# Kernel tuning notes

Measured on AMD Instinct MI355X. Metric: run time of the kernel, lower is better.

The kernel has to match this reference:

```python
import jax, jax.numpy as jnp
import numpy as np

C = 5.0          # tanh clamp constant (args.c, non-trainable)
B, N, R, D = 4, 16, 64, 256  # batch, block_num, block_len, word_dim
NEG = -1e9


def setup_inputs() -> dict:
    key = jax.random.key(0)
    ks = iter(jax.random.split(key, 80))

    def W(i, o):
        # xavier-like init (torch stores (out,in); we store (in,out) and use x @ W)
        return jax.random.normal(next(ks), (i, o), jnp.float32) * np.float32(np.sqrt(2.0 / (i + o)))

    def bvec(d):
        return jax.random.normal(next(ks), (d,), jnp.float32) * 0.01

    inp = {"x": jax.random.normal(next(ks), (B, N, R, D), jnp.float32)}
    for p in ("fw", "bw"):
        inp[f"fcW_{p}"] = W(D, D);  inp[f"fcb_{p}"] = bvec(D)
        inp[f"mW1_{p}"] = W(D, D);  inp[f"mW2_{p}"] = W(D, D);  inp[f"mb_{p}"] = bvec(D)
        inp[f"s2tW1_{p}"] = W(D, D); inp[f"s2tb1_{p}"] = bvec(D)
        inp[f"s2tW_{p}"] = W(D, D);  inp[f"s2tb_{p}"] = bvec(D)
        inp[f"gW1_{p}"] = W(D, D);  inp[f"gW2_{p}"] = W(D, D);  inp[f"gb_{p}"] = bvec(D)
        inp[f"fW1_{p}"] = W(3 * D, D); inp[f"fb1_{p}"] = bvec(D)
        inp[f"fW2_{p}"] = W(3 * D, D); inp[f"fb2_{p}"] = bvec(D)
    return inp


def _mSA(x, W1, W2, b, fw):
    # x: (..., L, d) -> (..., L, d). Additive per-feature attention with strict
    # triangular mask. fw: token i attends to j > i (last row zeroed);
    # bw: token i attends to j < i (first row zeroed). Matches the torch
    # -inf mask + narrow + zero-pad construction exactly.
    L = x.shape[-2]
    xi = (x @ W1)[..., :, None, :]                 # (..., L, 1, d)
    xj = (x @ W2)[..., None, :, :]                 # (..., 1, L, d)
    f = C * jnp.tanh((xi + xj + b) / C)            # (..., i, j, d)
    i = jnp.arange(L)[:, None]
    j = jnp.arange(L)[None, :]
    allowed = (j > i) if fw else (j < i)           # (L, L)
    scores = jnp.where(allowed[..., None], f, NEG)
    att = jax.nn.softmax(scores, axis=-2)          # softmax over j
    rowvalid = (jnp.arange(L) < L - 1) if fw else (jnp.arange(L) > 0)
    att = att * rowvalid[:, None, None].astype(x.dtype)
    return jnp.einsum('...ijd,...jd->...id', att, x)


def _s2t(x, W1, b1, Wo, bo):
    # source2token self-attention: (..., L, d) -> (..., d)
    f = jax.nn.relu(x @ W1 + b1)
    a = jax.nn.softmax(f @ Wo + bo, axis=-2)
    return jnp.sum(a * x, axis=-2)


def _mblosa(x, mW1, mW2, mb, s2tW1, s2tb1, s2tW, s2tb,
            gW1, gW2, gb, fW1, fb1, fW2, fb2, fw):
    Bb, n, r, d = x.shape
    h = _mSA(x, mW1, mW2, mb, fw)                  # (B, n, r, d) intra-block
    v = _s2t(h, s2tW1, s2tb1, s2tW, s2tb)          # (B, n, d)    block summary
    o = _mSA(v, mW1, mW2, mb, fw)                  # (B, n, d)    inter-block
    G = jax.nn.sigmoid(o @ gW1 + v @ gW2 + gb)
    e = G * o + (1.0 - G) * v                      # (B, n, d)
    # torch: cat of e[i] repeated r times, then narrow(1, 0, n)
    idx = jnp.arange(n) // r
    E = e[:, idx]                                  # (B, n, d)
    # torch: flatten blocks then narrow(1, 0, n) (faithful to source)
    xf = x.reshape(Bb, n * r, d)[:, :n]
    hf = h.reshape(Bb, n * r, d)[:, :n]
    cat = jnp.concatenate([xf, hf, E], axis=-1)    # (B, n, 3d)
    fusion = jax.nn.relu(cat @ fW1 + fb1)
    Gf = jax.nn.sigmoid(cat @ fW2 + fb2)
    return Gf * fusion + (1.0 - Gf) * xf           # (B, n, d)


def reference(x,
              fcW_fw, fcb_fw, mW1_fw, mW2_fw, mb_fw, s2tW1_fw, s2tb1_fw,
              s2tW_fw, s2tb_fw, gW1_fw, gW2_fw, gb_fw, fW1_fw, fb1_fw,
              fW2_fw, fb2_fw,
              fcW_bw, fcb_bw, mW1_bw, mW2_bw, mb_bw, s2tW1_bw, s2tb1_bw,
              s2tW_bw, s2tb_bw, gW1_bw, gW2_bw, gb_bw, fW1_bw, fb1_bw,
              fW2_bw, fb2_bw):
    in_fw = jax.nn.relu(x @ fcW_fw + fcb_fw)
    in_bw = jax.nn.relu(x @ fcW_bw + fcb_bw)
    u_fw = _mblosa(in_fw, mW1_fw, mW2_fw, mb_fw, s2tW1_fw, s2tb1_fw,
                   s2tW_fw, s2tb_fw, gW1_fw, gW2_fw, gb_fw,
                   fW1_fw, fb1_fw, fW2_fw, fb2_fw, True)
    u_bw = _mblosa(in_bw, mW1_bw, mW2_bw, mb_bw, s2tW1_bw, s2tb1_bw,
                   s2tW_bw, s2tb_bw, gW1_bw, gW2_bw, gb_bw,
                   fW1_bw, fb1_bw, fW2_bw, fb2_bw, False)
    return jnp.concatenate([u_fw, u_bw], axis=-1)  # (B, n, 2d)
```

## Files before the change

### kernel.cpp

```cpp
#include <hip/hip_runtime.h>
#include <hip/hip_bf16.h>

typedef __hip_bfloat16 BF16;
typedef __attribute__((ext_vector_type(8))) short short8;
typedef __attribute__((ext_vector_type(4))) float f32x4;

#define MFMA_B16(a,b,c) __builtin_amdgcn_mfma_f32_16x16x32_bf16((a),(b),(c),0,0,0)

#if __has_builtin(__builtin_amdgcn_exp2f)
#define EXP2F(x) __builtin_amdgcn_exp2f(x)
#else
#define EXP2F(x) __expf(0.6931471805599453f * (x))
#endif

__device__ __forceinline__ short f2bs(float f){ BF16 h = __float2bfloat16(f); return *(short*)&h; }
__device__ __forceinline__ float bs2f(short s){ BF16 h = *(BF16*)&s; return __bfloat162float(h); }

struct SrcPack { const float* s[10]; };

__global__ __launch_bounds__(256) void prep_k(SrcPack p, short* __restrict__ Oh,
                                              short* __restrict__ Ol)
{
    __shared__ float s[64][65];
    const float* W = p.s[blockIdx.y];
    short* oh = Oh + (size_t)blockIdx.y * 65536;
    short* ol = Ol + (size_t)blockIdx.y * 65536;
    int tr = (blockIdx.x >> 2) * 64, tc = (blockIdx.x & 3) * 64;
    #pragma unroll
    for (int i = 0; i < 16; i++) {
        int e = threadIdx.x + i * 256;
        int r = e >> 6, c = e & 63;
        s[c][r] = W[(size_t)(tr + r) * 256 + tc + c];
    }
    __syncthreads();
    #pragma unroll
    for (int i = 0; i < 16; i++) {
        int e = threadIdx.x + i * 256;
        int c2 = e >> 6, r2 = e & 63;
        float v = s[c2][r2];
        short hi = f2bs(v);
        short lo = f2bs(v - bs2f(hi));
        size_t oi = (size_t)(tc + c2) * 256 + tr + r2;
        oh[oi] = hi;
        ol[oi] = lo;
    }
}

template<int AM, int OM, int RELU, int BS>
__device__ __forceinline__ void gemm_body(const void* __restrict__ A0,
    const void* __restrict__ Alo,
    const short* __restrict__ Wh, const short* __restrict__ Wl,
    const float* __restrict__ bias, void* __restrict__ O0, void* __restrict__ O1,
    int row0, int col0)
{
    constexpr int LDK = 72;
    __shared__ short sAh[64 * LDK];
    __shared__ short sAl[(AM == 0) ? 8 : 64 * LDK];
    __shared__ short sBh[64 * LDK];
    __shared__ short sBl[BS ? 8 : 64 * LDK];
    int tid = threadIdx.x;
    int w = tid >> 6, l = tid & 63;
    int m = l & 15, q = l >> 4;
    int sr = w * 16 + m;

    f32x4 acc[4];
    #pragma unroll
    for (int cf = 0; cf < 4; cf++) acc[cf] = (f32x4)(0.f);

    for (int kh = 0; kh < 4; kh++) {
        int kbase = kh * 64;
        #pragma unroll
        for (int i = 0; i < 2; i++) {
            int kl = q * 8 + 32 * i;
            size_t gofs = (size_t)(row0 + sr) * 256 + kbase + kl;
            if (AM == 1) {
                const float* src = (const float*)A0 + gofs;
                float4 f0 = *(const float4*)src;
                float4 f1 = *(const float4*)(src + 4);
                short8 vh, vl;
                float tmp[8] = {f0.x, f0.y, f0.z, f0.w, f1.x, f1.y, f1.z, f1.w};
                #pragma unroll
                for (int j = 0; j < 8; j++) {
                    vh[j] = f2bs(tmp[j]);
                    vl[j] = f2bs(tmp[j] - bs2f(vh[j]));
                }
                *(short8*)&sAh[sr * LDK + kl] = vh;
                *(short8*)&sAl[sr * LDK + kl] = vl;
            } else if (AM == 2) {
                *(short8*)&sAh[sr * LDK + kl] = *(const short8*)((const short*)A0 + gofs);
                *(short8*)&sAl[sr * LDK + kl] = *(const short8*)((const short*)Alo + gofs);
            } else {
                *(short8*)&sAh[sr * LDK + kl] = *(const short8*)((const short*)A0 + gofs);
            }
            size_t gofsB = (size_t)(col0 + sr) * 256 + kbase + kl;
            *(short8*)&sBh[sr * LDK + kl] = *(const short8*)(Wh + gofsB);
            if (!BS)
                *(short8*)&sBl[sr * LDK + kl] = *(const short8*)(Wl + gofsB);
        }
        __syncthreads();
        #pragma unroll
        for (int ch = 0; ch < 2; ch++) {
            int k = ch * 32 + q * 8;
            short8 ah = *(const short8*)&sAh[(w * 16 + m) * LDK + k];
            short8 al = (AM != 0) ? *(const short8*)&sAl[(w * 16 + m) * LDK + k] : ah;
            #pragma unroll
            for (int cf = 0; cf < 4; cf++) {
                short8 bh = *(const short8*)&sBh[(cf * 16 + m) * LDK + k];
                acc[cf] = MFMA_B16(ah, bh, acc[cf]);
                if (!BS) {
                    short8 bl = *(const short8*)&sBl[(cf * 16 + m) * LDK + k];
                    acc[cf] = MFMA_B16(ah, bl, acc[cf]);
                }
                if (AM != 0)
                    acc[cf] = MFMA_B16(al, bh, acc[cf]);
            }
        }
        __syncthreads();
    }
    #pragma unroll
    for (int cf = 0; cf < 4; cf++) {
        int col = col0 + cf * 16 + m;
        float bv = bias ? bias[col] : 0.f;
        #pragma unroll
        for (int r = 0; r < 4; r++) {
            int row = row0 + w * 16 + q * 4 + r;
            float v = acc[cf][r] + bv;
            if (RELU) v = fmaxf(v, 0.f);
            size_t oi = (size_t)row * 256 + col;
            if (OM == 0) {
                ((float*)O0)[oi] = v;
            } else if (OM == 1) {
                ((short*)O0)[oi] = f2bs(v);
            } else {
                short hi = f2bs(v);
                ((short*)O0)[oi] = hi;
                ((short*)O1)[oi] = f2bs(v - bs2f(hi));
            }
        }
    }
}

struct GDir { const void* A0; const void* Al; const short* Wh; const short* Wl;
              const float* bias; void* O0; void* O1; };

template<int AM, int OM, int RELU, int BS>
__global__ __launch_bounds__(256) void gemm_k(GDir p0, GDir p1)
{
    GDir p = blockIdx.z ? p1 : p0;
    gemm_body<AM, OM, RELU, BS>(p.A0, p.Al, p.Wh, p.Wl, p.bias, p.O0, p.O1,
                                blockIdx.x * 64, blockIdx.y * 64);
}

struct G2Dir { const float* A; const short* W1h; const short* W1l;
               const short* W2h; const short* W2l; const float* b2;
               float* C1; float* C2; };

__global__ __launch_bounds__(256) void gemm2s_k(G2Dir p0)
{
    G2Dir p = p0;
    int y = blockIdx.y;
    const short* Wh = (y < 4) ? p.W1h : p.W2h;
    const short* Wl = (y < 4) ? p.W1l : p.W2l;
    void* C = (y < 4) ? (void*)p.C1 : (void*)p.C2;
    const float* bias = (y < 4) ? nullptr : p.b2;
    gemm_body<1, 0, 0, 0>(p.A, nullptr, Wh, Wl, bias, C, nullptr, 0, (y & 3) * 64);
}

struct MbloDir { const short* Ah;
                 const short* W1h; const short* W2h;
                 const float* mb; short* Hh; int fw; };

__global__ __launch_bounds__(512) void mblo_k(MbloDir p0, MbloDir p1)
{
    __shared__ char smraw[33536] __attribute__((aligned(16)));
    short* gAh  = (short*)smraw;
    short* gB1h = gAh + 4608;
    short* gB2h = gAh + 9216;
    float* aP   = (float*)smraw;
    unsigned int* aQX = (unsigned int*)(smraw + 16896);

    const float KLN = -0.06931471805599453f;

    MbloDir p = blockIdx.z ? p1 : p0;
    int tid = threadIdx.x;
    int w = tid >> 6, l = tid & 63;
    int m = l & 15, q = l >> 4;
    int rh = w >> 1;
    int cb = (w & 1) * 2;
    int bn = blockIdx.x >> 1, ipar = blockIdx.x & 1;
    int row0 = bn * 64, d0 = blockIdx.y * 64;
    int srow = tid >> 3;
    int skl  = (tid & 7) * 8;

    f32x4 acc1[2], acc2[2];
    #pragma unroll
    for (int cf = 0; cf < 2; cf++) { acc1[cf] = (f32x4)(0.f); acc2[cf] = (f32x4)(0.f); }

    for (int kh = 0; kh < 4; kh++) {
        int kbase = kh * 64;
        size_t ga = (size_t)(row0 + srow) * 256 + kbase + skl;
        *(short8*)&gAh[srow * 72 + skl] = *(const short8*)(p.Ah + ga);
        size_t gb = (size_t)(d0 + srow) * 256 + kbase + skl;
        *(short8*)&gB1h[srow * 72 + skl] = *(const short8*)(p.W1h + gb);
        *(short8*)&gB2h[srow * 72 + skl] = *(const short8*)(p.W2h + gb);
        __syncthreads();
        #pragma unroll
        for (int ch = 0; ch < 2; ch++) {
            int k = ch * 32 + q * 8;
            short8 ah = *(const short8*)&gAh[(rh * 16 + m) * 72 + k];
            #pragma unroll
            for (int cf = 0; cf < 2; cf++) {
                int bofs = ((cb + cf) * 16 + m) * 72 + k;
                short8 b1 = *(const short8*)&gB1h[bofs];
                acc1[cf] = MFMA_B16(ah, b1, acc1[cf]);
                short8 b2 = *(const short8*)&gB2h[bofs];
                acc2[cf] = MFMA_B16(ah, b2, acc2[cf]);
            }
        }
        __syncthreads();
    }
    short* sQX = (short*)aQX;
    #pragma unroll
    for (int cf = 0; cf < 2; cf++) {
        int col = (cb + cf) * 16 + m;
        float mbv = p.mb[d0 + col];
        #pragma unroll
        for (int r = 0; r < 4; r++) {
            int row = rh * 16 + q * 4 + r;
            aP[row * 66 + col] = __expf(0.4f * acc1[cf][r]) * KLN;
            sQX[col * 130 + 2 * row] = f2bs(__expf(0.4f * (acc2[cf][r] + mbv)));
        }
    }
    {
        size_t gx = (size_t)(row0 + srow) * 256 + d0 + skl;
        short8 xh = *(const short8*)(p.Ah + gx);
        #pragma unroll
        for (int t = 0; t < 8; t++)
            sQX[(skl + t) * 130 + 2 * srow + 1] = xh[t];
    }
    __syncthreads();
    const unsigned int* lane_qx = &aQX[l * 65];
    #pragma unroll
    for (int t8 = 0; t8 < 4; t8++) {
        int i = ipar + 2 * (w + 8 * t8);
        float Pp = aP[i * 66 + l];
        int js = p.fw ? (i + 1) : 0;
        int je = p.fw ? 64 : i;
        float den0 = 0.f, den1 = 0.f, num0 = 0.f, num1 = 0.f;
        int j = js;
        for (; j + 4 <= je; j += 4) {
            unsigned int u0 = lane_qx[j];
            unsigned int u1 = lane_qx[j + 1];
            unsigned int u2 = lane_qx[j + 2];
            unsigned int u3 = lane_qx[j + 3];
            float q0 = bs2f((short)(u0 & 0xffff)), x0 = bs2f((short)(u0 >> 16));
            float q1 = bs2f((short)(u1 & 0xffff)), x1 = bs2f((short)(u1 >> 16));
            float q2 = bs2f((short)(u2 & 0xffff)), x2 = bs2f((short)(u2 >> 16));
            float q3 = bs2f((short)(u3 & 0xffff)), x3 = bs2f((short)(u3 >> 16));
            float w0 = EXP2F(__builtin_amdgcn_rcpf(fmaf(Pp, q0, KLN)));
            float w1 = EXP2F(__builtin_amdgcn_rcpf(fmaf(Pp, q1, KLN)));
            float w2 = EXP2F(__builtin_amdgcn_rcpf(fmaf(Pp, q2, KLN)));
            float w3 = EXP2F(__builtin_amdgcn_rcpf(fmaf(Pp, q3, KLN)));
            den0 += w0; num0 = fmaf(w0, x0, num0);
            den1 += w1; num1 = fmaf(w1, x1, num1);
            den0 += w2; num0 = fmaf(w2, x2, num0);
            den1 += w3; num1 = fmaf(w3, x3, num1);
        }
        for (; j < je; j++) {
            unsigned int u0 = lane_qx[j];
            float q0 = bs2f((short)(u0 & 0xffff)), x0 = bs2f((short)(u0 >> 16));
            float wgt = EXP2F(__builtin_amdgcn_rcpf(fmaf(Pp, q0, KLN)));
            den0 += wgt; num0 = fmaf(wgt, x0, num0);
        }
        float den = den0 + den1, num = num0 + num1;
        bool valid = p.fw ? (i < 63) : (i > 0);
        float out = valid ? (num * __builtin_amdgcn_rcpf(den)) : 0.f;
        p.Hh[(size_t)(row0 + i) * 256 + d0 + l] = f2bs(out);
    }
}

struct PoolDir { const short* T1; const short* Wh; const float* bias;
                 const short* Hh; float* V; };

__global__ __launch_bounds__(256) void s2t_pool_k(PoolDir p0, PoolDir p1)
{
    __shared__ char smraw[37888] __attribute__((aligned(16)));
    short* gAh = (short*)smraw;
    short* gBh = gAh + 4608;
    float* aL = (float*)smraw;
    float* aH = aL + 4352;
    float* rm = aL + 8704;
    float* rd = aL + 8960;
    float* rn = aL + 9216;

    PoolDir p = blockIdx.z ? p1 : p0;
    int tid = threadIdx.x;
    int w = tid >> 6, l = tid & 63;
    int m = l & 15, q = l >> 4;
    int sr = w * 16 + m;
    int row0 = blockIdx.x * 64, d0 = blockIdx.y * 64;

    f32x4 acc[4];
    #pragma unroll
    for (int cf = 0; cf < 4; cf++) acc[cf] = (f32x4)(0.f);

    for (int kh = 0; kh < 4; kh++) {
        int kbase = kh * 64;
        #pragma unroll
        for (int i = 0; i < 2; i++) {
            int kl = q * 8 + 32 * i;
            *(short8*)&gAh[sr * 72 + kl] =
                *(const short8*)(p.T1 + (size_t)(row0 + sr) * 256 + kbase + kl);
            *(short8*)&gBh[sr * 72 + kl] =
                *(const short8*)(p.Wh + (size_t)(d0 + sr) * 256 + kbase + kl);
        }
        __syncthreads();
        #pragma unroll
        for (int ch = 0; ch < 2; ch++) {
            int k = ch * 32 + q * 8;
            short8 ah = *(const short8*)&gAh[(w * 16 + m) * 72 + k];
            #pragma unroll
            for (int cf = 0; cf < 4; cf++) {
                short8 bh = *(const short8*)&gBh[(cf * 16 + m) * 72 + k];
                acc[cf] = MFMA_B16(ah, bh, acc[cf]);
            }
        }
        __syncthreads();
    }
    #pragma unroll
    for (int cf = 0; cf < 4; cf++) {
        int col = cf * 16 + m;
        float bv = p.bias[d0 + col];
        #pragma unroll
        for (int r = 0; r < 4; r++) {
            int row = w * 16 + q * 4 + r;
            aL[row * 68 + col] = acc[cf][r] + bv;
        }
    }
    #pragma unroll
    for (int it = 0; it < 2; it++) {
        int e = tid + it * 256;
        int j = e >> 3, d8 = (e & 7) * 8;
        short8 xh = *(const short8*)(p.Hh + (size_t)(row0 + j) * 256 + d0 + d8);
        #pragma unroll
        for (int t = 0; t < 8; t++)
            aH[j * 68 + d8 + t] = bs2f(xh[t]);
    }
    __syncthreads();
    int dl = tid & 63, rq = tid >> 6;
    float mx = -1e30f, den = 0.f, num = 0.f;
    #pragma unroll
    for (int rr = 0; rr < 16; rr++) {
        int r = rq * 16 + rr;
        float lv = aL[r * 68 + dl];
        float hv = aH[r * 68 + dl];
        if (lv > mx) {
            float sc = __expf(mx - lv);
            den *= sc; num *= sc; mx = lv;
        }
        float wgt = __expf(lv - mx);
        den += wgt; num += wgt * hv;
    }
    rm[rq * 64 + dl] = mx; rd[rq * 64 + dl] = den; rn[rq * 64 + dl] = num;
    __syncthreads();
    if (rq == 0) {
        float M = fmaxf(fmaxf(rm[dl], rm[64 + dl]), fmaxf(rm[128 + dl], rm[192 + dl]));
        float D = 0.f, Nn = 0.f;
        #pragma unroll
        for (int k = 0; k < 4; k++) {
            float sc = __expf(rm[k * 64 + dl] - M);
            D += rd[k * 64 + dl] * sc;
            Nn += rn[k * 64 + dl] * sc;
        }
        p.V[(size_t)blockIdx.x * 256 + d0 + dl] = Nn / D;
    }
}

struct GateDir { const float* vW1; const float* vW2; const float* V;
                 const float* gW1; const float* gW2; const float* gb;
                 float* E0; int fw; };

__global__ __launch_bounds__(256) void attn2gate_k(GateDir p0, GateDir p1)
{
    GateDir p = blockIdx.z ? p1 : p0;
    __shared__ float so[256], sv[256], red[4][64];
    int b = blockIdx.x, k = threadIdx.x;
    float o = 0.f;
    if (p.fw) {
        float qv = p.vW1[(size_t)(b * 16) * 256 + k];
        float den = 0.f, num = 0.f;
        for (int j = 1; j < 16; j++) {
            float z = (qv + p.vW2[(size_t)(b * 16 + j) * 256 + k]) * 0.2f;
            float e2 = __expf(2.f * z);
            float t = 1.f - 2.f / (e2 + 1.f);
            float wgt = __expf(5.f * t);
            den += wgt; num += wgt * p.V[(size_t)(b * 16 + j) * 256 + k];
        }
        o = num / den;
    }
    so[k] = o;
    sv[k] = p.V[(size_t)(b * 16) * 256 + k];
    __syncthreads();
    int c = k & 63, ks = k >> 6;
    int gc = blockIdx.y * 64 + c;
    float acc = 0.f;
    int k0 = ks * 64;
    #pragma unroll 8
    for (int kk = 0; kk < 64; kk++) {
        int kx = k0 + kk;
        acc += so[kx] * p.gW1[(size_t)kx * 256 + gc] + sv[kx] * p.gW2[(size_t)kx * 256 + gc];
    }
    red[ks][c] = acc;
    __syncthreads();
    if (ks == 0) {
        float a = red[0][c] + red[1][c] + red[2][c] + red[3][c] + p.gb[gc];
        float G = 1.f / (1.f + __expf(-a));
        p.E0[b * 256 + gc] = G * so[gc] + (1.f - G) * sv[gc];
    }
}

struct FuseDir { const short* INh; const short* Hh;
                 const float* E0; const float* fW1; const float* fb1;
                 const float* fW2; const float* fb2; };

__global__ __launch_bounds__(256) void fusion_k(FuseDir p0, FuseDir p1, float* __restrict__ out)
{
    FuseDir p = blockIdx.z ? p1 : p0;
    __shared__ float cat[768];
    __shared__ float red1[4][64], red2[4][64];
    int bt = blockIdx.x, b = bt >> 4, t = bt & 15;
    int c = threadIdx.x & 63, ks = threadIdx.x >> 6;
    int gc = blockIdx.y * 64 + c;
    size_t xrow = ((size_t)b * 1024 + t) * 256;
    cat[threadIdx.x]       = bs2f(p.INh[xrow + threadIdx.x]);
    cat[256 + threadIdx.x] = bs2f(p.Hh[xrow + threadIdx.x]);
    cat[512 + threadIdx.x] = p.E0[b * 256 + threadIdx.x];
    __syncthreads();
    float a1 = 0.f, a2 = 0.f;
    int k0 = ks * 192;
    #pragma unroll 8
    for (int kk = 0; kk < 192; kk++) {
        int k = k0 + kk;
        float cv = cat[k];
        a1 += cv * p.fW1[(size_t)k * 256 + gc];
        a2 += cv * p.fW2[(size_t)k * 256 + gc];
    }
    red1[ks][c] = a1; red2[ks][c] = a2;
    __syncthreads();
    if (ks == 0) {
        float s1 = red1[0][c] + red1[1][c] + red1[2][c] + red1[3][c] + p.fb1[gc];
        float s2 = red2[0][c] + red2[1][c] + red2[2][c] + red2[3][c] + p.fb2[gc];
        float fus = fmaxf(s1, 0.f);
        float Gf = 1.f / (1.f + __expf(-s2));
        float u = Gf * fus + (1.f - Gf) * cat[gc];
        out[((size_t)(b * 16 + t)) * 512 + (size_t)blockIdx.z * 256 + gc] = u;
    }
}

extern "C" void kernel_launch(void* const* d_in, const int* in_sizes, int n_in,
                              void* d_out, int out_size, void* d_ws, size_t ws_size,
                              hipStream_t stream)
{
    const float* x = (const float*)d_in[0];
    char* base = (char*)d_ws;
    auto alloc = [&](size_t bytes){ void* r = base; base += (bytes + 255) & ~255ULL; return r; };
    short* inH = (short*)alloc(2 * 1048576 * 2);
    short* hH  = (short*)alloc(2 * 1048576 * 2);
    short* t1  = (short*)alloc(2 * 1048576 * 2);
    short* wtH = (short*)alloc(10 * 65536 * 2);
    short* wtL = (short*)alloc(10 * 65536 * 2);
    float* v   = (float*)alloc(2 * 16384 * 4);
    float* vW1 = (float*)alloc(16384 * 4);
    float* vW2 = (float*)alloc(16384 * 4);
    float* E0  = (float*)alloc(2 * 1024 * 4);

    SrcPack sp;
    const int src_idx[5] = {0, 2, 3, 5, 7};
    for (int p = 0; p < 2; p++)
        for (int i = 0; i < 5; i++)
            sp.s[p * 5 + i] = (const float*)d_in[1 + p * 16 + src_idx[i]];
    prep_k<<<dim3(16, 10), 256, 0, stream>>>(sp, wtH, wtL);

    GDir fc[2], s2t1[2];
    MbloDir mbd[2];
    PoolDir pld[2];
    G2Dir g2d;
    GateDir gtd[2];
    FuseDir fsd[2];
    for (int p = 0; p < 2; p++) {
        int bi = 1 + p * 16;
        const float* fcb   = (const float*)d_in[bi + 1];
        const float* mb    = (const float*)d_in[bi + 4];
        const float* s2tb1 = (const float*)d_in[bi + 6];
        const float* s2tb  = (const float*)d_in[bi + 8];
        size_t po = (size_t)p * 1048576;
        const short* W0h = wtH + (size_t)(p * 5 + 0) * 65536, *W0l = wtL + (size_t)(p * 5 + 0) * 65536;
        const short* W1h = wtH + (size_t)(p * 5 + 1) * 65536, *W1l = wtL + (size_t)(p * 5 + 1) * 65536;
        const short* W2h = wtH + (size_t)(p * 5 + 2) * 65536, *W2l = wtL + (size_t)(p * 5 + 2) * 65536;
        const short* W3h = wtH + (size_t)(p * 5 + 3) * 65536;
        const short* W4h = wtH + (size_t)(p * 5 + 4) * 65536;

        fc[p]   = { x, nullptr, W0h, W0l, fcb, inH + po, nullptr };
        mbd[p]  = { inH + po, W1h, W2h, mb, hH + po, (p == 0) };
        s2t1[p] = { hH + po, nullptr, W3h, nullptr, s2tb1, t1 + po, nullptr };
        pld[p]  = { t1 + po, W4h, s2tb, hH + po, v + p * 16384 };
        if (p == 0) g2d = { v, W1h, W1l, W2h, W2l, mb, vW1, vW2 };
        gtd[p]  = { vW1, vW2, v + p * 16384,
                    (const float*)d_in[bi + 9], (const float*)d_in[bi + 10],
                    (const float*)d_in[bi + 11], E0 + p * 1024, (p == 0) };
        fsd[p]  = { inH + po, hH + po, E0 + p * 1024,
                    (const float*)d_in[bi + 12], (const float*)d_in[bi + 13],
                    (const float*)d_in[bi + 14], (const float*)d_in[bi + 15] };
    }

    gemm_k<1, 1, 1, 0><<<dim3(64, 4, 2), 256, 0, stream>>>(fc[0], fc[1]);
    mblo_k<<<dim3(128, 4, 2), 512, 0, stream>>>(mbd[0], mbd[1]);
    gemm_k<0, 1, 1, 1><<<dim3(64, 4, 2), 256, 0, stream>>>(s2t1[0], s2t1[1]);
    s2t_pool_k<<<dim3(64, 4, 2), 256, 0, stream>>>(pld[0], pld[1]);
    gemm2s_k<<<dim3(1, 8, 1), 256, 0, stream>>>(g2d);
    attn2gate_k<<<dim3(4, 4, 2), 256, 0, stream>>>(gtd[0], gtd[1]);
    fusion_k<<<dim3(64, 4, 2), 256, 0, stream>>>(fsd[0], fsd[1], (float*)d_out);
}
```

Baseline: 200.8 us.

## Fuse s2t GEMM into pooling kernel and fold inter-block projections into gate kernel

The s2t first GEMM (ReLU) is now computed per 64-row block inside the pooling kernel, with T1 kept in shared memory, so the t1 global buffer and one launch go away. Each block recomputes T1 for its two output column chunks, so that GEMM runs twice across blockIdx.y. The separate gemm2s kernel that projected V through W1/W2 is removed. Those projections are now computed in fp32 directly inside attn2gate using the original weights, which cuts two launches in total and adds redundant per-block scalar FMA work.

```diff
diff --git a/kernel.cpp b/kernel.cpp
--- a/kernel.cpp
+++ b/kernel.cpp
@@ -149,21 +149,6 @@
     GDir p = blockIdx.z ? p1 : p0;
     gemm_body<AM, OM, RELU, BS>(p.A0, p.Al, p.Wh, p.Wl, p.bias, p.O0, p.O1,
                                 blockIdx.x * 64, blockIdx.y * 64);
-}
-
-struct G2Dir { const float* A; const short* W1h; const short* W1l;
-               const short* W2h; const short* W2l; const float* b2;
-               float* C1; float* C2; };
-
-__global__ __launch_bounds__(256) void gemm2s_k(G2Dir p0)
-{
-    G2Dir p = p0;
-    int y = blockIdx.y;
-    const short* Wh = (y < 4) ? p.W1h : p.W2h;
-    const short* Wl = (y < 4) ? p.W1l : p.W2l;
-    void* C = (y < 4) ? (void*)p.C1 : (void*)p.C2;
-    const float* bias = (y < 4) ? nullptr : p.b2;
-    gemm_body<1, 0, 0, 0>(p.A, nullptr, Wh, Wl, bias, C, nullptr, 0, (y & 3) * 64);
 }
 
 struct MbloDir { const short* Ah;
@@ -279,141 +264,222 @@
     }
 }
 
-struct PoolDir { const short* T1; const short* Wh; const float* bias;
-                 const short* Hh; float* V; };
-
-__global__ __launch_bounds__(256) void s2t_pool_k(PoolDir p0, PoolDir p1)
-{
-    __shared__ char smraw[37888] __attribute__((aligned(16)));
-    short* gAh = (short*)smraw;
-    short* gBh = gAh + 4608;
-    float* aL = (float*)smraw;
-    float* aH = aL + 4352;
-    float* rm = aL + 8704;
-    float* rd = aL + 8960;
-    float* rn = aL + 9216;
-
-    PoolDir p = blockIdx.z ? p1 : p0;
+struct S2TDir { const short* Hh; const short* W3h; const float* b1;
+                const short* W4h; const float* b2; float* V; };
+
+__global__ __launch_bounds__(512) void s2t_fused_k(S2TDir p0, S2TDir p1)
+{
+    __shared__ char smraw[79872] __attribute__((aligned(16)));
+    short* sT1 = (short*)smraw;
+    short* gA  = (short*)(smraw + 33792);
+    short* gB  = (short*)(smraw + 43008);
+    short* gB2 = (short*)(smraw + 33792);
+    float* aL  = (float*)(smraw + 43008);
+    float* rm  = (float*)(smraw + 60416);
+    float* rd  = rm + 512;
+    float* rn  = rm + 1024;
+
+    S2TDir p = blockIdx.z ? p1 : p0;
     int tid = threadIdx.x;
     int w = tid >> 6, l = tid & 63;
     int m = l & 15, q = l >> 4;
-    int sr = w * 16 + m;
-    int row0 = blockIdx.x * 64, d0 = blockIdx.y * 64;
-
-    f32x4 acc[4];
-    #pragma unroll
-    for (int cf = 0; cf < 4; cf++) acc[cf] = (f32x4)(0.f);
-
+    int row0 = blockIdx.x * 64;
+    int strip = w >> 1, chalf = w & 1;
+    int srow = tid >> 3, skl = (tid & 7) * 8;
+
+    f32x4 acc1[8];
+    #pragma unroll
+    for (int cf = 0; cf < 8; cf++) acc1[cf] = (f32x4)(0.f);
     for (int kh = 0; kh < 4; kh++) {
         int kbase = kh * 64;
-        #pragma unroll
-        for (int i = 0; i < 2; i++) {
-            int kl = q * 8 + 32 * i;
-            *(short8*)&gAh[sr * 72 + kl] =
-                *(const short8*)(p.T1 + (size_t)(row0 + sr) * 256 + kbase + kl);
-            *(short8*)&gBh[sr * 72 + kl] =
-                *(const short8*)(p.Wh + (size_t)(d0 + sr) * 256 + kbase + kl);
+        *(short8*)&gA[srow * 72 + skl] =
+            *(const short8*)(p.Hh + (size_t)(row0 + srow) * 256 + kbase + skl);
+        int bn = tid >> 1;
+        #pragma unroll
+        for (int i = 0; i < 4; i++) {
+            int kseg = (tid & 1) * 32 + i * 8;
+            *(short8*)&gB[bn * 72 + kseg] =
+                *(const short8*)(p.W3h + (size_t)bn * 256 + kbase + kseg);
         }
         __syncthreads();
         #pragma unroll
         for (int ch = 0; ch < 2; ch++) {
             int k = ch * 32 + q * 8;
-            short8 ah = *(const short8*)&gAh[(w * 16 + m) * 72 + k];
-            #pragma unroll
-            for (int cf = 0; cf < 4; cf++) {
-                short8 bh = *(const short8*)&gBh[(cf * 16 + m) * 72 + k];
-                acc[cf] = MFMA_B16(ah, bh, acc[cf]);
-            }
-        }
-        __syncthreads();
-    }
-    #pragma unroll
-    for (int cf = 0; cf < 4; cf++) {
-        int col = cf * 16 + m;
-        float bv = p.bias[d0 + col];
+            short8 ah = *(const short8*)&gA[(strip * 16 + m) * 72 + k];
+            #pragma unroll
+            for (int cf = 0; cf < 8; cf++) {
+                short8 bh = *(const short8*)&gB[(chalf * 128 + cf * 16 + m) * 72 + k];
+                acc1[cf] = MFMA_B16(ah, bh, acc1[cf]);
+            }
+        }
+        __syncthreads();
+    }
+    #pragma unroll
+    for (int cf = 0; cf < 8; cf++) {
+        int col = chalf * 128 + cf * 16 + m;
+        float bv = p.b1[col];
         #pragma unroll
         for (int r = 0; r < 4; r++) {
-            int row = w * 16 + q * 4 + r;
-            aL[row * 68 + col] = acc[cf][r] + bv;
-        }
-    }
-    #pragma unroll
-    for (int it = 0; it < 2; it++) {
-        int e = tid + it * 256;
-        int j = e >> 3, d8 = (e & 7) * 8;
-        short8 xh = *(const short8*)(p.Hh + (size_t)(row0 + j) * 256 + d0 + d8);
-        #pragma unroll
-        for (int t = 0; t < 8; t++)
-            aH[j * 68 + d8 + t] = bs2f(xh[t]);
-    }
-    __syncthreads();
-    int dl = tid & 63, rq = tid >> 6;
-    float mx = -1e30f, den = 0.f, num = 0.f;
-    #pragma unroll
-    for (int rr = 0; rr < 16; rr++) {
-        int r = rq * 16 + rr;
-        float lv = aL[r * 68 + dl];
-        float hv = aH[r * 68 + dl];
-        if (lv > mx) {
-            float sc = __expf(mx - lv);
-            den *= sc; num *= sc; mx = lv;
-        }
-        float wgt = __expf(lv - mx);
-        den += wgt; num += wgt * hv;
-    }
-    rm[rq * 64 + dl] = mx; rd[rq * 64 + dl] = den; rn[rq * 64 + dl] = num;
-    __syncthreads();
-    if (rq == 0) {
-        float M = fmaxf(fmaxf(rm[dl], rm[64 + dl]), fmaxf(rm[128 + dl], rm[192 + dl]));
-        float D = 0.f, Nn = 0.f;
-        #pragma unroll
-        for (int k = 0; k < 4; k++) {
-            float sc = __expf(rm[k * 64 + dl] - M);
-            D += rd[k * 64 + dl] * sc;
-            Nn += rn[k * 64 + dl] * sc;
-        }
-        p.V[(size_t)blockIdx.x * 256 + d0 + dl] = Nn / D;
-    }
-}
-
-struct GateDir { const float* vW1; const float* vW2; const float* V;
-                 const float* gW1; const float* gW2; const float* gb;
-                 float* E0; int fw; };
-
-__global__ __launch_bounds__(256) void attn2gate_k(GateDir p0, GateDir p1)
-{
-    GateDir p = blockIdx.z ? p1 : p0;
-    __shared__ float so[256], sv[256], red[4][64];
-    int b = blockIdx.x, k = threadIdx.x;
-    float o = 0.f;
+            int row = strip * 16 + q * 4 + r;
+            sT1[row * 264 + col] = f2bs(fmaxf(acc1[cf][r] + bv, 0.f));
+        }
+    }
+    __syncthreads();
+
+    for (int dc = 0; dc < 2; dc++) {
+        int d0 = (blockIdx.y * 2 + dc) * 64;
+        f32x4 acc2[2];
+        acc2[0] = (f32x4)(0.f); acc2[1] = (f32x4)(0.f);
+        for (int kh = 0; kh < 4; kh++) {
+            int kbase = kh * 64;
+            *(short8*)&gB2[srow * 72 + skl] =
+                *(const short8*)(p.W4h + (size_t)(d0 + srow) * 256 + kbase + skl);
+            __syncthreads();
+            #pragma unroll
+            for (int ch = 0; ch < 2; ch++) {
+                int k = ch * 32 + q * 8;
+                short8 ah = *(const short8*)&sT1[(strip * 16 + m) * 264 + kbase + k];
+                #pragma unroll
+                for (int cf = 0; cf < 2; cf++) {
+                    short8 bh = *(const short8*)&gB2[(chalf * 32 + cf * 16 + m) * 72 + k];
+                    acc2[cf] = MFMA_B16(ah, bh, acc2[cf]);
+                }
+            }
+            __syncthreads();
+        }
+        #pragma unroll
+        for (int cf = 0; cf < 2; cf++) {
+            int col = chalf * 32 + cf * 16 + m;
+            float bv = p.b2[d0 + col];
+            #pragma unroll
+            for (int r = 0; r < 4; r++) {
+                int row = strip * 16 + q * 4 + r;
+                aL[row * 68 + col] = acc2[cf][r] + bv;
+            }
+        }
+        __syncthreads();
+        int dl = tid & 63, rq = tid >> 6;
+        float mx = -1e30f, den = 0.f, num = 0.f;
+        #pragma unroll
+        for (int rr = 0; rr < 8; rr++) {
+            int r = rq * 8 + rr;
+            float lv = aL[r * 68 + dl];
+            float hv = bs2f(p.Hh[(size_t)(row0 + r) * 256 + d0 + dl]);
+            if (lv > mx) { float sc = __expf(mx - lv); den *= sc; num *= sc; mx = lv; }
+            float wgt = __expf(lv - mx);
+            den += wgt; num = fmaf(wgt, hv, num);
+        }
+        rm[rq * 64 + dl] = mx; rd[rq * 64 + dl] = den; rn[rq * 64 + dl] = num;
+        __syncthreads();
+        if (rq == 0) {
+            float M = rm[dl];
+            #pragma unroll
+            for (int kq = 1; kq < 8; kq++) M = fmaxf(M, rm[kq * 64 + dl]);
+            float D = 0.f, Nn = 0.f;
+            #pragma unroll
+            for (int kq = 0; kq < 8; kq++) {
+                float sc = __expf(rm[kq * 64 + dl] - M);
+                D += rd[kq * 64 + dl] * sc;
+                Nn += rn[kq * 64 + dl] * sc;
+            }
+            p.V[(size_t)blockIdx.x * 256 + d0 + dl] = Nn / D;
+        }
+        __syncthreads();
+    }
+}
+
+struct Gate2Dir { const float* V; const float* W1; const float* W2; const float* mb;
+                  const float* gW1; const float* gW2; const float* gb;
+                  float* E0; int fw; };
+
+__global__ __launch_bounds__(512) void attn2gate_k(Gate2Dir p0, Gate2Dir p1)
+{
+    Gate2Dir p = blockIdx.z ? p1 : p0;
+    __shared__ __attribute__((aligned(16))) float sVT[4096];
+    __shared__ float sPart[16][256];
+    __shared__ float so[256], sv[256], red[8][64];
+    int tid = threadIdx.x;
+    int b = blockIdx.x;
+    int k = tid & 255, half = tid >> 8;
+
     if (p.fw) {
-        float qv = p.vW1[(size_t)(b * 16) * 256 + k];
-        float den = 0.f, num = 0.f;
-        for (int j = 1; j < 16; j++) {
-            float z = (qv + p.vW2[(size_t)(b * 16 + j) * 256 + k]) * 0.2f;
-            float e2 = __expf(2.f * z);
-            float t = 1.f - 2.f / (e2 + 1.f);
-            float wgt = __expf(5.f * t);
-            den += wgt; num += wgt * p.V[(size_t)(b * 16 + j) * 256 + k];
-        }
-        o = num / den;
-    }
-    so[k] = o;
-    sv[k] = p.V[(size_t)(b * 16) * 256 + k];
-    __syncthreads();
-    int c = k & 63, ks = k >> 6;
+        #pragma unroll
+        for (int it = 0; it < 8; it++) {
+            int e = tid + it * 512;
+            int kk = e >> 4, j = e & 15;
+            sVT[e] = p.V[(size_t)(b * 16 + j) * 256 + kk];
+        }
+        __syncthreads();
+        float acc[16];
+        #pragma unroll
+        for (int j = 0; j < 16; j++) acc[j] = 0.f;
+        int kk0 = half * 128;
+        #pragma unroll 4
+        for (int kk = kk0; kk < kk0 + 128; kk++) {
+            const float4* vr = (const float4*)&sVT[kk * 16];
+            float4 va = vr[0], vb = vr[1], vc = vr[2], vd = vr[3];
+            float w1 = p.W1[(size_t)kk * 256 + k];
+            float w2 = p.W2[(size_t)kk * 256 + k];
+            acc[0]  = fmaf(va.x, w1, acc[0]);
+            acc[1]  = fmaf(va.y, w2, acc[1]);
+            acc[2]  = fmaf(va.z, w2, acc[2]);
+            acc[3]  = fmaf(va.w, w2, acc[3]);
+            acc[4]  = fmaf(vb.x, w2, acc[4]);
+            acc[5]  = fmaf(vb.y, w2, acc[5]);
+            acc[6]  = fmaf(vb.z, w2, acc[6]);
+            acc[7]  = fmaf(vb.w, w2, acc[7]);
+            acc[8]  = fmaf(vc.x, w2, acc[8]);
+            acc[9]  = fmaf(vc.y, w2, acc[9]);
+            acc[10] = fmaf(vc.z, w2, acc[10]);
+            acc[11] = fmaf(vc.w, w2, acc[11]);
+            acc[12] = fmaf(vd.x, w2, acc[12]);
+            acc[13] = fmaf(vd.y, w2, acc[13]);
+            acc[14] = fmaf(vd.z, w2, acc[14]);
+            acc[15] = fmaf(vd.w, w2, acc[15]);
+        }
+        if (half) {
+            #pragma unroll
+            for (int j = 0; j < 16; j++) sPart[j][k] = acc[j];
+        }
+        __syncthreads();
+        if (!half) {
+            #pragma unroll
+            for (int j = 0; j < 16; j++) acc[j] += sPart[j][k];
+            float base = acc[0] + p.mb[k];
+            float den = 0.f, num = 0.f;
+            #pragma unroll
+            for (int j = 1; j < 16; j++) {
+                float z = (base + acc[j]) * 0.2f;
+                float e2 = __expf(2.f * z);
+                float t = 1.f - 2.f / (e2 + 1.f);
+                float wgt = __expf(5.f * t);
+                den += wgt;
+                num = fmaf(wgt, p.V[(size_t)(b * 16 + j) * 256 + k], num);
+            }
+            so[k] = num / den;
+            sv[k] = p.V[(size_t)(b * 16) * 256 + k];
+        }
+    } else {
+        if (!half) {
+            so[k] = 0.f;
+            sv[k] = p.V[(size_t)(b * 16) * 256 + k];
+        }
+    }
+    __syncthreads();
+    int c = tid & 63, ks = tid >> 6;
     int gc = blockIdx.y * 64 + c;
-    float acc = 0.f;
-    int k0 = ks * 64;
+    float a2 = 0.f;
+    int k0 = ks * 32;
     #pragma unroll 8
-    for (int kk = 0; kk < 64; kk++) {
-        int kx = k0 + kk;
-        acc += so[kx] * p.gW1[(size_t)kx * 256 + gc] + sv[kx] * p.gW2[(size_t)kx * 256 + gc];
-    }
-    red[ks][c] = acc;
+    for (int kkx = 0; kkx < 32; kkx++) {
+        int kx = k0 + kkx;
+        a2 += so[kx] * p.gW1[(size_t)kx * 256 + gc] + sv[kx] * p.gW2[(size_t)kx * 256 + gc];
+    }
+    red[ks][c] = a2;
     __syncthreads();
     if (ks == 0) {
-        float a = red[0][c] + red[1][c] + red[2][c] + red[3][c] + p.gb[gc];
+        float a = red[0][c] + red[1][c] + red[2][c] + red[3][c]
+                + red[4][c] + red[5][c] + red[6][c] + red[7][c] + p.gb[gc];
         float G = 1.f / (1.f + __expf(-a));
         p.E0[b * 256 + gc] = G * so[gc] + (1.f - G) * sv[gc];
     }
@@ -466,12 +532,9 @@
     auto alloc = [&](size_t bytes){ void* r = base; base += (bytes + 255) & ~255ULL; return r; };
     short* inH = (short*)alloc(2 * 1048576 * 2);
     short* hH  = (short*)alloc(2 * 1048576 * 2);
-    short* t1  = (short*)alloc(2 * 1048576 * 2);
     short* wtH = (short*)alloc(10 * 65536 * 2);
     short* wtL = (short*)alloc(10 * 65536 * 2);
     float* v   = (float*)alloc(2 * 16384 * 4);
-    float* vW1 = (float*)alloc(16384 * 4);
-    float* vW2 = (float*)alloc(16384 * 4);
     float* E0  = (float*)alloc(2 * 1024 * 4);
 
     SrcPack sp;
@@ -481,11 +544,10 @@
             sp.s[p * 5 + i] = (const float*)d_in[1 + p * 16 + src_idx[i]];
     prep_k<<<dim3(16, 10), 256, 0, stream>>>(sp, wtH, wtL);
 
-    GDir fc[2], s2t1[2];
+    GDir fc[2];
     MbloDir mbd[2];
-    PoolDir pld[2];
-    G2Dir g2d;
-    GateDir gtd[2];
+    S2TDir std[2];
+    Gate2Dir gtd[2];
     FuseDir fsd[2];
     for (int p = 0; p < 2; p++) {
         int bi = 1 + p * 16;
@@ -495,17 +557,16 @@
         const float* s2tb  = (const float*)d_in[bi + 8];
         size_t po = (size_t)p * 1048576;
         const short* W0h = wtH + (size_t)(p * 5 + 0) * 65536, *W0l = wtL + (size_t)(p * 5 + 0) * 65536;
-        const short* W1h = wtH + (size_t)(p * 5 + 1) * 65536, *W1l = wtL + (size_t)(p * 5 + 1) * 65536;
-        const short* W2h = wtH + (size_t)(p * 5 + 2) * 65536, *W2l = wtL + (size_t)(p * 5 + 2) * 65536;
+        const short* W1h = wtH + (size_t)(p * 5 + 1) * 65536;
+        const short* W2h = wtH + (size_t)(p * 5 + 2) * 65536;
         const short* W3h = wtH + (size_t)(p * 5 + 3) * 65536;
         const short* W4h = wtH + (size_t)(p * 5 + 4) * 65536;
 
         fc[p]   = { x, nullptr, W0h, W0l, fcb, inH + po, nullptr };
         mbd[p]  = { inH + po, W1h, W2h, mb, hH + po, (p == 0) };
-        s2t1[p] = { hH + po, nullptr, W3h, nullptr, s2tb1, t1 + po, nullptr };
-        pld[p]  = { t1 + po, W4h, s2tb, hH + po, v + p * 16384 };
-        if (p == 0) g2d = { v, W1h, W1l, W2h, W2l, mb, vW1, vW2 };
-        gtd[p]  = { vW1, vW2, v + p * 16384,
+        std[p]  = { hH + po, W3h, s2tb1, W4h, s2tb, v + p * 16384 };
+        gtd[p]  = { v + p * 16384,
+                    (const float*)d_in[bi + 2], (const float*)d_in[bi + 3], mb,
                     (const float*)d_in[bi + 9], (const float*)d_in[bi + 10],
                     (const float*)d_in[bi + 11], E0 + p * 1024, (p == 0) };
         fsd[p]  = { inH + po, hH + po, E0 + p * 1024,
@@ -515,9 +576,7 @@
 
     gemm_k<1, 1, 1, 0><<<dim3(64, 4, 2), 256, 0, stream>>>(fc[0], fc[1]);
     mblo_k<<<dim3(128, 4, 2), 512, 0, stream>>>(mbd[0], mbd[1]);
-    gemm_k<0, 1, 1, 1><<<dim3(64, 4, 2), 256, 0, stream>>>(s2t1[0], s2t1[1]);
-    s2t_pool_k<<<dim3(64, 4, 2), 256, 0, stream>>>(pld[0], pld[1]);
-    gemm2s_k<<<dim3(1, 8, 1), 256, 0, stream>>>(g2d);
-    attn2gate_k<<<dim3(4, 4, 2), 256, 0, stream>>>(gtd[0], gtd[1]);
+    s2t_fused_k<<<dim3(64, 2, 2), 512, 0, stream>>>(std[0], std[1]);
+    attn2gate_k<<<dim3(4, 4, 2), 512, 0, stream>>>(gtd[0], gtd[1]);
     fusion_k<<<dim3(64, 4, 2), 256, 0, stream>>>(fsd[0], fsd[1], (float*)d_out);
 }
```

Measured after the change: 207.8 us. 1.03x slower.

## Fuse small attention projection GEMM into gate kernel and pre-split x to bf16

Applied to the files above, without the earlier changes.

Removes the separate gemm2s kernel and computes the V@W1/V@W2 projections in fp32 inside attn2gate_k, which now uses 512 threads with a split-K reduction through shared memory. x is converted once into hi/lo bf16 arrays in the prep kernel, so the fc GEMM reads pre-split operands instead of converting fp32 per direction. This saves one launch and the duplicate conversion of x, but each gate block recomputes the projection redundantly and the prep kernel does extra work.

```diff
diff --git a/kernel.cpp b/kernel.cpp
--- a/kernel.cpp
+++ b/kernel.cpp
@@ -3,6 +3,7 @@
 
 typedef __hip_bfloat16 BF16;
 typedef __attribute__((ext_vector_type(8))) short short8;
+typedef __attribute__((ext_vector_type(4))) short short4v;
 typedef __attribute__((ext_vector_type(4))) float f32x4;
 
 #define MFMA_B16(a,b,c) __builtin_amdgcn_mfma_f32_16x16x32_bf16((a),(b),(c),0,0,0)
@@ -18,9 +19,31 @@
 
 struct SrcPack { const float* s[10]; };
 
-__global__ __launch_bounds__(256) void prep_k(SrcPack p, short* __restrict__ Oh,
-                                              short* __restrict__ Ol)
-{
+__global__ __launch_bounds__(256) void prep_k(SrcPack p, const float* __restrict__ X,
+                                              short* __restrict__ Oh,
+                                              short* __restrict__ Ol,
+                                              short* __restrict__ Xh,
+                                              short* __restrict__ Xl)
+{
+    if (blockIdx.y >= 10) {
+        int u = (blockIdx.y - 10) * 16 + blockIdx.x;
+        size_t base = (size_t)u * 16384;
+        #pragma unroll
+        for (int i = 0; i < 16; i++) {
+            size_t idx = base + (size_t)i * 1024 + threadIdx.x * 4;
+            float4 f = *(const float4*)(X + idx);
+            short4v vh, vl;
+            float t0[4] = {f.x, f.y, f.z, f.w};
+            #pragma unroll
+            for (int j = 0; j < 4; j++) {
+                vh[j] = f2bs(t0[j]);
+                vl[j] = f2bs(t0[j] - bs2f(vh[j]));
+            }
+            *(short4v*)(Xh + idx) = vh;
+            *(short4v*)(Xl + idx) = vl;
+        }
+        return;
+    }
     __shared__ float s[64][65];
     const float* W = p.s[blockIdx.y];
     short* oh = Oh + (size_t)blockIdx.y * 65536;
@@ -50,7 +73,7 @@
 __device__ __forceinline__ void gemm_body(const void* __restrict__ A0,
     const void* __restrict__ Alo,
     const short* __restrict__ Wh, const short* __restrict__ Wl,
-    const float* __restrict__ bias, void* __restrict__ O0, void* __restrict__ O1,
+    const float* __restrict__ bias, void* __restrict__ O0,
     int row0, int col0)
 {
     constexpr int LDK = 72;
@@ -73,20 +96,7 @@
         for (int i = 0; i < 2; i++) {
             int kl = q * 8 + 32 * i;
             size_t gofs = (size_t)(row0 + sr) * 256 + kbase + kl;
-            if (AM == 1) {
-                const float* src = (const float*)A0 + gofs;
-                float4 f0 = *(const float4*)src;
-                float4 f1 = *(const float4*)(src + 4);
-                short8 vh, vl;
-                float tmp[8] = {f0.x, f0.y, f0.z, f0.w, f1.x, f1.y, f1.z, f1.w};
-                #pragma unroll
-                for (int j = 0; j < 8; j++) {
-                    vh[j] = f2bs(tmp[j]);
-                    vl[j] = f2bs(tmp[j] - bs2f(vh[j]));
-                }
-                *(short8*)&sAh[sr * LDK + kl] = vh;
-                *(short8*)&sAl[sr * LDK + kl] = vl;
-            } else if (AM == 2) {
+            if (AM == 2) {
                 *(short8*)&sAh[sr * LDK + kl] = *(const short8*)((const short*)A0 + gofs);
                 *(short8*)&sAl[sr * LDK + kl] = *(const short8*)((const short*)Alo + gofs);
             } else {
@@ -129,41 +139,22 @@
             size_t oi = (size_t)row * 256 + col;
             if (OM == 0) {
                 ((float*)O0)[oi] = v;
-            } else if (OM == 1) {
+            } else {
                 ((short*)O0)[oi] = f2bs(v);
-            } else {
-                short hi = f2bs(v);
-                ((short*)O0)[oi] = hi;
-                ((short*)O1)[oi] = f2bs(v - bs2f(hi));
             }
         }
     }
 }
 
 struct GDir { const void* A0; const void* Al; const short* Wh; const short* Wl;
-              const float* bias; void* O0; void* O1; };
+              const float* bias; void* O0; };
 
 template<int AM, int OM, int RELU, int BS>
 __global__ __launch_bounds__(256) void gemm_k(GDir p0, GDir p1)
 {
     GDir p = blockIdx.z ? p1 : p0;
-    gemm_body<AM, OM, RELU, BS>(p.A0, p.Al, p.Wh, p.Wl, p.bias, p.O0, p.O1,
+    gemm_body<AM, OM, RELU, BS>(p.A0, p.Al, p.Wh, p.Wl, p.bias, p.O0,
                                 blockIdx.x * 64, blockIdx.y * 64);
-}
-
-struct G2Dir { const float* A; const short* W1h; const short* W1l;
-               const short* W2h; const short* W2l; const float* b2;
-               float* C1; float* C2; };
-
-__global__ __launch_bounds__(256) void gemm2s_k(G2Dir p0)
-{
-    G2Dir p = p0;
-    int y = blockIdx.y;
-    const short* Wh = (y < 4) ? p.W1h : p.W2h;
-    const short* Wl = (y < 4) ? p.W1l : p.W2l;
-    void* C = (y < 4) ? (void*)p.C1 : (void*)p.C2;
-    const float* bias = (y < 4) ? nullptr : p.b2;
-    gemm_body<1, 0, 0, 0>(p.A, nullptr, Wh, Wl, bias, C, nullptr, 0, (y & 3) * 64);
 }
 
 struct MbloDir { const short* Ah;
@@ -376,44 +367,98 @@
     }
 }
 
-struct GateDir { const float* vW1; const float* vW2; const float* V;
-                 const float* gW1; const float* gW2; const float* gb;
-                 float* E0; int fw; };
-
-__global__ __launch_bounds__(256) void attn2gate_k(GateDir p0, GateDir p1)
-{
-    GateDir p = blockIdx.z ? p1 : p0;
-    __shared__ float so[256], sv[256], red[4][64];
-    int b = blockIdx.x, k = threadIdx.x;
-    float o = 0.f;
+struct Gate2Dir { const float* V; const float* W1; const float* W2; const float* mb;
+                  const float* gW1; const float* gW2; const float* gb;
+                  float* E0; int fw; };
+
+__global__ __launch_bounds__(512) void attn2gate_k(Gate2Dir p0, Gate2Dir p1)
+{
+    Gate2Dir p = blockIdx.z ? p1 : p0;
+    __shared__ __attribute__((aligned(16))) float sVT[4096];
+    __shared__ float sPart[16][256];
+    __shared__ float so[256], sv[256], red[8][64];
+    int tid = threadIdx.x;
+    int b = blockIdx.x;
+    int k = tid & 255, half = tid >> 8;
+
     if (p.fw) {
-        float qv = p.vW1[(size_t)(b * 16) * 256 + k];
-        float den = 0.f, num = 0.f;
-        for (int j = 1; j < 16; j++) {
-            float z = (qv + p.vW2[(size_t)(b * 16 + j) * 256 + k]) * 0.2f;
-            float e2 = __expf(2.f * z);
-            float t = 1.f - 2.f / (e2 + 1.f);
-            float wgt = __expf(5.f * t);
-            den += wgt; num += wgt * p.V[(size_t)(b * 16 + j) * 256 + k];
-        }
-        o = num / den;
-    }
-    so[k] = o;
-    sv[k] = p.V[(size_t)(b * 16) * 256 + k];
-    __syncthreads();
-    int c = k & 63, ks = k >> 6;
+        #pragma unroll
+        for (int it = 0; it < 8; it++) {
+            int e = tid + it * 512;
+            int kk = e >> 4, j = e & 15;
+            sVT[e] = p.V[(size_t)(b * 16 + j) * 256 + kk];
+        }
+        __syncthreads();
+        float acc[16];
+        #pragma unroll
+        for (int j = 0; j < 16; j++) acc[j] = 0.f;
+        int kk0 = half * 128;
+        #pragma unroll 4
+        for (int kk = kk0; kk < kk0 + 128; kk++) {
+            const float4* vr = (const float4*)&sVT[kk * 16];
+            float4 va = vr[0], vb = vr[1], vc = vr[2], vd = vr[3];
+            float w1 = p.W1[(size_t)kk * 256 + k];
+            float w2 = p.W2[(size_t)kk * 256 + k];
+            acc[0]  = fmaf(va.x, w1, acc[0]);
+            acc[1]  = fmaf(va.y, w2, acc[1]);
+            acc[2]  = fmaf(va.z, w2, acc[2]);
+            acc[3]  = fmaf(va.w, w2, acc[3]);
+            acc[4]  = fmaf(vb.x, w2, acc[4]);
+            acc[5]  = fmaf(vb.y, w2, acc[5]);
+            acc[6]  = fmaf(vb.z, w2, acc[6]);
+            acc[7]  = fmaf(vb.w, w2, acc[7]);
+            acc[8]  = fmaf(vc.x, w2, acc[8]);
+            acc[9]  = fmaf(vc.y, w2, acc[9]);
+            acc[10] = fmaf(vc.z, w2, acc[10]);
+            acc[11] = fmaf(vc.w, w2, acc[11]);
+            acc[12] = fmaf(vd.x, w2, acc[12]);
+            acc[13] = fmaf(vd.y, w2, acc[13]);
+            acc[14] = fmaf(vd.z, w2, acc[14]);
+            acc[15] = fmaf(vd.w, w2, acc[15]);
+        }
+        if (half) {
+            #pragma unroll
+            for (int j = 0; j < 16; j++) sPart[j][k] = acc[j];
+        }
+        __syncthreads();
+        if (!half) {
+            #pragma unroll
+            for (int j = 0; j < 16; j++) acc[j] += sPart[j][k];
+            float base = acc[0] + p.mb[k];
+            float den = 0.f, num = 0.f;
+            #pragma unroll
+            for (int j = 1; j < 16; j++) {
+                float z = (base + acc[j]) * 0.2f;
+                float e2 = __expf(2.f * z);
+                float t = 1.f - 2.f / (e2 + 1.f);
+                float wgt = __expf(5.f * t);
+                den += wgt;
+                num = fmaf(wgt, p.V[(size_t)(b * 16 + j) * 256 + k], num);
+            }
+            so[k] = num / den;
+            sv[k] = p.V[(size_t)(b * 16) * 256 + k];
+        }
+    } else {
+        if (!half) {
+            so[k] = 0.f;
+            sv[k] = p.V[(size_t)(b * 16) * 256 + k];
+        }
+    }
+    __syncthreads();
+    int c = tid & 63, ks = tid >> 6;
     int gc = blockIdx.y * 64 + c;
-    float acc = 0.f;
-    int k0 = ks * 64;
+    float a2 = 0.f;
+    int k0 = ks * 32;
     #pragma unroll 8
-    for (int kk = 0; kk < 64; kk++) {
-        int kx = k0 + kk;
-        acc += so[kx] * p.gW1[(size_t)kx * 256 + gc] + sv[kx] * p.gW2[(size_t)kx * 256 + gc];
-    }
-    red[ks][c] = acc;
+    for (int kkx = 0; kkx < 32; kkx++) {
+        int kx = k0 + kkx;
+        a2 += so[kx] * p.gW1[(size_t)kx * 256 + gc] + sv[kx] * p.gW2[(size_t)kx * 256 + gc];
+    }
+    red[ks][c] = a2;
     __syncthreads();
     if (ks == 0) {
-        float a = red[0][c] + red[1][c] + red[2][c] + red[3][c] + p.gb[gc];
+        float a = red[0][c] + red[1][c] + red[2][c] + red[3][c]
+                + red[4][c] + red[5][c] + red[6][c] + red[7][c] + p.gb[gc];
         float G = 1.f / (1.f + __expf(-a));
         p.E0[b * 256 + gc] = G * so[gc] + (1.f - G) * sv[gc];
     }
@@ -469,9 +514,9 @@
     short* t1  = (short*)alloc(2 * 1048576 * 2);
     short* wtH = (short*)alloc(10 * 65536 * 2);
     short* wtL = (short*)alloc(10 * 65536 * 2);
+    short* xh  = (short*)alloc(1048576 * 2);
+    short* xl  = (short*)alloc(1048576 * 2);
     float* v   = (float*)alloc(2 * 16384 * 4);
-    float* vW1 = (float*)alloc(16384 * 4);
-    float* vW2 = (float*)alloc(16384 * 4);
     float* E0  = (float*)alloc(2 * 1024 * 4);
 
     SrcPack sp;
@@ -479,13 +524,12 @@
     for (int p = 0; p < 2; p++)
         for (int i = 0; i < 5; i++)
             sp.s[p * 5 + i] = (const float*)d_in[1 + p * 16 + src_idx[i]];
-    prep_k<<<dim3(16, 10), 256, 0, stream>>>(sp, wtH, wtL);
+    prep_k<<<dim3(16, 14), 256, 0, stream>>>(sp, x, wtH, wtL, xh, xl);
 
     GDir fc[2], s2t1[2];
     MbloDir mbd[2];
     PoolDir pld[2];
-    G2Dir g2d;
-    GateDir gtd[2];
+    Gate2Dir gtd[2];
     FuseDir fsd[2];
     for (int p = 0; p < 2; p++) {
         int bi = 1 + p * 16;
@@ -495,17 +539,17 @@
         const float* s2tb  = (const float*)d_in[bi + 8];
         size_t po = (size_t)p * 1048576;
         const short* W0h = wtH + (size_t)(p * 5 + 0) * 65536, *W0l = wtL + (size_t)(p * 5 + 0) * 65536;
-        const short* W1h = wtH + (size_t)(p * 5 + 1) * 65536, *W1l = wtL + (size_t)(p * 5 + 1) * 65536;
-        const short* W2h = wtH + (size_t)(p * 5 + 2) * 65536, *W2l = wtL + (size_t)(p * 5 + 2) * 65536;
+        const short* W1h = wtH + (size_t)(p * 5 + 1) * 65536;
+        const short* W2h = wtH + (size_t)(p * 5 + 2) * 65536;
         const short* W3h = wtH + (size_t)(p * 5 + 3) * 65536;
         const short* W4h = wtH + (size_t)(p * 5 + 4) * 65536;
 
-        fc[p]   = { x, nullptr, W0h, W0l, fcb, inH + po, nullptr };
+        fc[p]   = { xh, xl, W0h, W0l, fcb, inH + po };
         mbd[p]  = { inH + po, W1h, W2h, mb, hH + po, (p == 0) };
-        s2t1[p] = { hH + po, nullptr, W3h, nullptr, s2tb1, t1 + po, nullptr };
+        s2t1[p] = { hH + po, nullptr, W3h, nullptr, s2tb1, t1 + po };
         pld[p]  = { t1 + po, W4h, s2tb, hH + po, v + p * 16384 };
-        if (p == 0) g2d = { v, W1h, W1l, W2h, W2l, mb, vW1, vW2 };
-        gtd[p]  = { vW1, vW2, v + p * 16384,
+        gtd[p]  = { v + p * 16384,
+                    (const float*)d_in[bi + 2], (const float*)d_in[bi + 3], mb,
                     (const float*)d_in[bi + 9], (const float*)d_in[bi + 10],
                     (const float*)d_in[bi + 11], E0 + p * 1024, (p == 0) };
         fsd[p]  = { inH + po, hH + po, E0 + p * 1024,
@@ -513,11 +557,10 @@
                     (const float*)d_in[bi + 14], (const float*)d_in[bi + 15] };
     }
 
-    gemm_k<1, 1, 1, 0><<<dim3(64, 4, 2), 256, 0, stream>>>(fc[0], fc[1]);
+    gemm_k<2, 1, 1, 0><<<dim3(64, 4, 2), 256, 0, stream>>>(fc[0], fc[1]);
     mblo_k<<<dim3(128, 4, 2), 512, 0, stream>>>(mbd[0], mbd[1]);
     gemm_k<0, 1, 1, 1><<<dim3(64, 4, 2), 256, 0, stream>>>(s2t1[0], s2t1[1]);
     s2t_pool_k<<<dim3(64, 4, 2), 256, 0, stream>>>(pld[0], pld[1]);
-    gemm2s_k<<<dim3(1, 8, 1), 256, 0, stream>>>(g2d);
-    attn2gate_k<<<dim3(4, 4, 2), 256, 0, stream>>>(gtd[0], gtd[1]);
+    attn2gate_k<<<dim3(4, 4, 2), 512, 0, stream>>>(gtd[0], gtd[1]);
     fusion_k<<<dim3(64, 4, 2), 256, 0, stream>>>(fsd[0], fsd[1], (float*)d_out);
 }
```

New measurement: 211.4 us. 1.05x slower.
